# Kernel tuning notes

Measured on AMD Instinct MI355X. Metric: run time of the kernel, lower is better.

Reference implementation:

```python
import jax, jax.numpy as jnp
from jax import lax
import numpy as np


def conv4d(x, w, b, pad):
    """4D conv (stride 1) as a sum of 3D convs over the first-spatial-dim kernel taps.
    x: [B, Cin, T, D, H, W]; w: [Cout, Cin, Kt, Kd, Kh, Kw]; same pad on all dims."""
    B, Cin, T, D, H, W = x.shape
    Cout, _, Kt = w.shape[:3]
    xp = jnp.pad(x, ((0, 0), (0, 0), (pad, pad), (0, 0), (0, 0), (0, 0)))
    Tout = T + 2 * pad - Kt + 1
    acc = None
    for k in range(Kt):  # loop over kernel taps (<=3), not data dims
        xs = xp[:, :, k:k + Tout]                      # [B,Cin,Tout,D,H,W]
        xs = xs.transpose(0, 2, 1, 3, 4, 5).reshape(B * Tout, Cin, D, H, W)
        y = lax.conv_general_dilated(
            xs, w[:, :, k], (1, 1, 1), [(pad, pad)] * 3,
            dimension_numbers=('NCDHW', 'OIDHW', 'NCDHW'))
        acc = y if acc is None else acc + y
    Do, Ho, Wo = acc.shape[2:]
    out = acc.reshape(B, Tout, Cout, Do, Ho, Wo).transpose(0, 2, 1, 3, 4, 5)
    return out + b[None, :, None, None, None, None]


def tconv4d_k2s2(x, w, b):
    """4D transposed conv, kernel=2, stride=2, pad=0 (non-overlapping blocks).
    x: [B,Cin,T,D,H,W]; w: [Cin,Cout,2,2,2,2] (PyTorch ConvTranspose layout)."""
    B, Cin, T, D, H, W = x.shape
    Cout = w.shape[1]
    y = jnp.einsum('bcijkl,copqrs->boipjqkrls', x, w)
    y = y.reshape(B, Cout, 2 * T, 2 * D, 2 * H, 2 * W)
    return y + b[None, :, None, None, None, None]


def setup_inputs() -> dict:
    key = jax.random.key(0)
    ks = jax.random.split(key, 10)
    Cin, Cout = 64, 32
    x1 = jax.random.normal(ks[0], (2, Cin, 8, 8, 8, 8), dtype=jnp.float32)
    x2 = jax.random.normal(ks[1], (2, Cin // 2, 16, 16, 16, 16), dtype=jnp.float32)
    def w(k, shape, fan_in):
        return jax.random.normal(k, shape, dtype=jnp.float32) / np.float32(np.sqrt(fan_in))
    up_w = w(ks[2], (Cin, Cin // 2, 2, 2, 2, 2), Cin * 16)
    up_b = w(ks[3], (Cin // 2,), Cin * 16)
    w1 = w(ks[4], (Cout, Cin, 3, 3, 3, 3), Cin * 81)
    b1 = w(ks[5], (Cout,), Cin * 81)
    w2 = w(ks[6], (Cout, Cout, 3, 3, 3, 3), Cout * 81)
    b2 = w(ks[7], (Cout,), Cout * 81)
    w3 = w(ks[8], (Cout, Cin, 1, 1, 1, 1), Cin)
    b3 = w(ks[9], (Cout,), Cin)
    return {'x1': x1, 'x2': x2, 'up_w': up_w, 'up_b': up_b,
            'w1': w1, 'b1': b1, 'w2': w2, 'b2': b2, 'w3': w3, 'b3': b3}


def reference(x1, x2, up_w, up_b, w1, b1, w2, b2, w3, b3):
    x1u = tconv4d_k2s2(x1, up_w, up_b)              # [B, Cin//2, 16,16,16,16]
    xc = jnp.concatenate([x2, x1u], axis=1)          # [B, Cin, 16,16,16,16]
    Y = jax.nn.relu(conv4d(xc, w1, b1, 1))
    Y = conv4d(Y, w2, b2, 1)
    sc = conv4d(xc, w3, b3, 0)                       # 1x1 residual projection
    return jax.nn.relu(Y + sc)
```

## Files before the change

kernel.cpp:

```cpp
#include <hip/hip_runtime.h>

typedef unsigned short u16;
typedef __attribute__((ext_vector_type(8))) short short8;
typedef __attribute__((ext_vector_type(4))) float f32x4;

#define XCB_OFF  0
#define Y1B_OFF  8388608
#define W1P_OFF  12582912
#define W2P_OFF  12748800
#define W3P_OFF  12831744
#define UPWP_OFF 12833792
#define X1T_OFF  12866560

__device__ __forceinline__ u16 f2bf(float v) {
    unsigned u = __builtin_bit_cast(unsigned, v);
    u += 0x7FFFu + ((u >> 16) & 1u);
    return (u16)(u >> 16);
}

__device__ __forceinline__ f32x4 MFMA(short8 a, short8 b, f32x4 c) {
    return __builtin_amdgcn_mfma_f32_16x16x32_bf16(a, b, c, 0, 0, 0);
}

__device__ __forceinline__ void decode_bid(int bid, int& b, int& t, int& d, int& h0) {
    int xcd = bid & 7, loc = bid >> 3;
    int hB = loc & 1;
    d = (loc >> 1) & 15;
    int tsub = (loc >> 5) & 1;
    b = loc >> 6;
    t = xcd * 2 + tsub;
    h0 = hB * 8;
}

__global__ __launch_bounds__(256) void setup(const float* __restrict__ w1,
                                             const float* __restrict__ w2,
                                             const float* __restrict__ w3,
                                             const float* __restrict__ upw,
                                             const float* __restrict__ x1,
                                             const float* __restrict__ x2,
                                             u16* __restrict__ ws) {
    __shared__ u16 lds[256 * 72];
    int bid = blockIdx.x;
    int tid = threadIdx.x;
    if (bid < 32) {
        int b = bid >> 4;
        int pos_base = (bid & 15) * 256;
        u16* x1t = ws + X1T_OFF;
        #pragma unroll
        for (int c = 0; c < 64; ++c) {
            lds[tid * 72 + c] = f2bf(x1[((b * 64 + c) << 12) + pos_base + tid]);
        }
        __syncthreads();
        #pragma unroll
        for (int k = 0; k < 8; ++k) {
            int f = k * 256 + tid;
            int u = f & 7, pos = f >> 3;
            uint4 v = *(const uint4*)(lds + pos * 72 + u * 8);
            *(uint4*)(x1t + (size_t)((b << 12) + pos_base + pos) * 64 + u * 8) = v;
        }
    } else if (bid < 544) {
        int lb = bid - 32;
        int b = lb >> 8;
        int pos_base = (lb & 255) * 256;
        u16* xcb = ws + XCB_OFF;
        #pragma unroll
        for (int c = 0; c < 32; ++c) {
            lds[tid * 40 + c] = f2bf(x2[((b * 32 + c) << 16) + pos_base + tid]);
        }
        __syncthreads();
        #pragma unroll
        for (int k = 0; k < 4; ++k) {
            int f = k * 256 + tid;
            int u = f & 3, pos = f >> 2;
            uint4 v = *(const uint4*)(lds + pos * 40 + u * 8);
            *(uint4*)(xcb + (size_t)((b << 16) + pos_base + pos) * 64 + u * 8) = v;
        }
    } else {
        int idx = (bid - 544) * 256 + tid;
        if (idx < 165888) {
            int j = idx & 7, lane = (idx >> 3) & 63, rest = idx >> 9;
            int half = rest & 1, chunk = (rest >> 1) & 1, tap = rest >> 2;
            int co = half * 16 + (lane & 15), ci = chunk * 32 + (lane >> 4) * 8 + j;
            ws[W1P_OFF + idx] = f2bf(w1[(co * 64 + ci) * 81 + tap]);
        } else if (idx < 165888 + 82944) {
            int i2 = idx - 165888;
            int j = i2 & 7, lane = (i2 >> 3) & 63, rest = i2 >> 9;
            int half = rest & 1, tap = rest >> 1;
            int co = half * 16 + (lane & 15), ci = (lane >> 4) * 8 + j;
            ws[W2P_OFF + i2] = f2bf(w2[(co * 32 + ci) * 81 + tap]);
        } else if (idx < 165888 + 82944 + 2048) {
            int i3 = idx - (165888 + 82944);
            int j = i3 & 7, lane = (i3 >> 3) & 63, rest = i3 >> 9;
            int half = rest & 1, chunk = rest >> 1;
            int co = half * 16 + (lane & 15), ci = chunk * 32 + (lane >> 4) * 8 + j;
            ws[W3P_OFF + i3] = f2bf(w3[co * 64 + ci]);
        } else if (idx < 250880 + 32768) {
            int i4 = idx - 250880;
            int j = i4 & 7, lane = (i4 >> 3) & 63, rest = i4 >> 9;
            int half = rest & 1, chunk = (rest >> 1) & 1, tap = rest >> 2;
            int co = half * 16 + (lane & 15), ci = chunk * 32 + (lane >> 4) * 8 + j;
            ws[UPWP_OFF + i4] = f2bf(upw[(ci * 32 + co) * 16 + tap]);
        }
    }
}

__global__ __launch_bounds__(256) void xc_up_mfma(const u16* __restrict__ x1t,
                                                  const u16* __restrict__ upwp,
                                                  const float* __restrict__ up_b,
                                                  u16* __restrict__ xcb) {
    int tid = threadIdx.x;
    int wv = tid >> 6, lane = tid & 63;
    int q = lane >> 4, m = lane & 15;
    int wid = blockIdx.x * 4 + wv;
    int j = wid & 63, tap = (wid >> 6) & 15, b = wid >> 10;

    f32x4 acc[4][2];
    {
        float4 bi0 = ((const float4*)up_b)[q];
        float4 bi1 = ((const float4*)up_b)[4 + q];
        #pragma unroll
        for (int g = 0; g < 4; ++g) {
            acc[g][0] = (f32x4){bi0.x, bi0.y, bi0.z, bi0.w};
            acc[g][1] = (f32x4){bi1.x, bi1.y, bi1.z, bi1.w};
        }
    }

    const short8* wv8 = (const short8*)upwp;
    const u16* xb = x1t + (size_t)((b << 12) + (j << 6) + m) * 64;
    #pragma unroll
    for (int chunk = 0; chunk < 2; ++chunk) {
        short8 a0 = wv8[((tap * 2 + chunk) * 2 + 0) * 64 + lane];
        short8 a1 = wv8[((tap * 2 + chunk) * 2 + 1) * 64 + lane];
        #pragma unroll
        for (int g = 0; g < 4; ++g) {
            short8 bf = *(const short8*)(xb + (size_t)(g * 16) * 64 + chunk * 32 + q * 8);
            acc[g][0] = MFMA(a0, bf, acc[g][0]);
            acc[g][1] = MFMA(a1, bf, acc[g][1]);
        }
    }

    int it = j >> 3, id = j & 7;
    int pt = tap >> 3, pd = (tap >> 2) & 1, ph = (tap >> 1) & 1, pw = tap & 1;
    int oT = 2 * it + pt, oD = 2 * id + pd, oW = 2 * (m & 7) + pw;
    #pragma unroll
    for (int g = 0; g < 4; ++g) {
        int ih = g * 2 + (m >> 3);
        int opos = oT * 4096 + oD * 256 + (2 * ih + ph) * 16 + oW;
        u16* op = xcb + (size_t)((b << 16) + opos) * 64 + 32 + q * 4;
        #pragma unroll
        for (int half = 0; half < 2; ++half) {
            f32x4 v = acc[g][half];
            uint2 o;
            o.x = (unsigned)f2bf(v.x) | ((unsigned)f2bf(v.y) << 16);
            o.y = (unsigned)f2bf(v.z) | ((unsigned)f2bf(v.w) << 16);
            *(uint2*)(op + half * 16) = o;
        }
    }
}

__global__ __launch_bounds__(256, 4) void conv1_mfma(const u16* __restrict__ xcb,
                                                     const u16* __restrict__ w1p,
                                                     const float* __restrict__ b1,
                                                     u16* __restrict__ y1b) {
    __shared__ u16 lds[11520];
    int tid = threadIdx.x;
    int lane = tid & 63, wv = tid >> 6;
    int q = lane >> 4, m = lane & 15;
    int c = wv & 1, rg = wv >> 1;
    int b, t, d, h0;
    decode_bid(blockIdx.x, b, t, d, h0);
    int rot = (blockIdx.x * 5) % 9;

    int lofs[6], gofs[6];
    bool st[6], inr[6];
    #pragma unroll
    for (int k = 0; k < 6; ++k) {
        int ui = tid + k * 256;
        int u = ui & 7, p = (ui >> 3) % 18, hh = ui / 144;
        int gh = h0 - 1 + hh, gw = p - 1;
        st[k] = ui < 1440;
        inr[k] = st[k] && ((unsigned)gh < 16u) && ((unsigned)gw < 16u);
        gofs[k] = (gh * 16 + gw) * 64 + u * 8;
        lofs[k] = hh * 1152 + p * 64 + ((u ^ (p & 7)) * 8);
    }

    f32x4 acc[4][2];
    if (c == 0) {
        float4 bi0 = ((const float4*)b1)[q];
        float4 bi1 = ((const float4*)b1)[4 + q];
        #pragma unroll
        for (int i = 0; i < 4; ++i) {
            acc[i][0] = (f32x4){bi0.x, bi0.y, bi0.z, bi0.w};
            acc[i][1] = (f32x4){bi1.x, bi1.y, bi1.z, bi1.w};
        }
    } else {
        #pragma unroll
        for (int i = 0; i < 4; ++i) {
            acc[i][0] = (f32x4){0.f, 0.f, 0.f, 0.f};
            acc[i][1] = (f32x4){0.f, 0.f, 0.f, 0.f};
        }
    }
    const short8* w1v = (const short8*)w1p;

    uint4 rP[6];
    auto load_plane = [&](int ktd) {
        int kt = ktd / 3, kd = ktd - kt * 3;
        int tt = t + kt - 1, dd = d + kd - 1;
        bool pv = ((unsigned)tt < 16u) && ((unsigned)dd < 16u);
        const u16* src = xcb + (size_t)(((b * 16 + tt) * 16 + dd)) * 16384;
        #pragma unroll
        for (int k = 0; k < 6; ++k) {
            uint4 v = {0, 0, 0, 0};
            if (pv && inr[k]) v = *(const uint4*)(src + gofs[k]);
            rP[k] = v;
        }
    };
    auto write_plane = [&]() {
        #pragma unroll
        for (int k = 0; k < 6; ++k)
            if (st[k]) *(uint4*)(lds + lofs[k]) = rP[k];
    };

    load_plane(rot);
    for (int s = 0; s < 9; ++s) {
        int ktd = rot + s; if (ktd >= 9) ktd -= 9;
        __syncthreads();
        write_plane();
        if (s < 8) {
            int nk = ktd + 1; if (nk >= 9) nk -= 9;
            load_plane(nk);
        }
        __syncthreads();
        __builtin_amdgcn_s_setprio(1);
        #pragma unroll
        for (int kw = 0; kw < 3; ++kw) {
            int p = kw + m, pm = p & 7;
            int bo = p * 64 + ((((c << 2) | q) ^ pm) << 3);
            short8 R[6];
            #pragma unroll
            for (int r = 0; r < 6; ++r)
                R[r] = *(const short8*)(lds + (rg * 4 + r) * 1152 + bo);
            #pragma unroll
            for (int kh = 0; kh < 3; ++kh) {
                int tap = (ktd * 3 + kh) * 3 + kw;
                short8 a0 = w1v[((tap * 2 + c) * 2 + 0) * 64 + lane];
                short8 a1 = w1v[((tap * 2 + c) * 2 + 1) * 64 + lane];
                #pragma unroll
                for (int i = 0; i < 4; ++i) {
                    acc[i][0] = MFMA(a0, R[i + kh], acc[i][0]);
                    acc[i][1] = MFMA(a1, R[i + kh], acc[i][1]);
                }
            }
        }
        __builtin_amdgcn_s_setprio(0);
    }

    __syncthreads();
    f32x4* buf = (f32x4*)lds;
    if (c == 1) {
        #pragma unroll
        for (int i = 0; i < 4; ++i)
            #pragma unroll
            for (int half = 0; half < 2; ++half)
                buf[((rg * 4 + i) * 2 + half) * 64 + lane] = acc[i][half];
    }
    __syncthreads();
    if (c == 0) {
        int obase = ((b * 16 + t) * 16 + d) * 256 + (h0 + rg * 4) * 16 + m;
        #pragma unroll
        for (int i = 0; i < 4; ++i) {
            int pos = obase + i * 16;
            #pragma unroll
            for (int half = 0; half < 2; ++half) {
                f32x4 v = acc[i][half];
                f32x4 w = buf[((rg * 4 + i) * 2 + half) * 64 + lane];
                v.x += w.x; v.y += w.y; v.z += w.z; v.w += w.w;
                unsigned r0 = f2bf(fmaxf(v.x, 0.f)), r1 = f2bf(fmaxf(v.y, 0.f));
                unsigned r2 = f2bf(fmaxf(v.z, 0.f)), r3 = f2bf(fmaxf(v.w, 0.f));
                uint2 o;
                o.x = r0 | (r1 << 16);
                o.y = r2 | (r3 << 16);
                *(uint2*)(y1b + (size_t)pos * 32 + half * 16 + q * 4) = o;
            }
        }
    }
}

__global__ __launch_bounds__(256, 2) void conv2_mfma(const u16* __restrict__ y1b,
                                                     const u16* __restrict__ xcb,
                                                     const u16* __restrict__ w2p,
                                                     const u16* __restrict__ w3p,
                                                     const float* __restrict__ b2,
                                                     const float* __restrict__ b3,
                                                     float* __restrict__ out) {
    __shared__ u16 lds[2][10368];
    int tid = threadIdx.x;
    int lane = tid & 63, wv = tid >> 6;
    int q = lane >> 4, m = lane & 15;
    int rg = wv;
    int bid = blockIdx.x;
    int xcd = bid & 7, loc = bid >> 3;
    int d = loc & 15;
    int tsub = (loc >> 4) & 1;
    int b = loc >> 5;
    int t = xcd * 2 + tsub;
    int rot = (bid * 5) % 9;

    int lofs[6], gofs[6];
    bool st[6], inr[6];
    #pragma unroll
    for (int k = 0; k < 6; ++k) {
        int ui = tid + k * 256;
        int u = ui & 3, p = (ui >> 2) % 18, hh = ui / 72;
        int gh = hh - 1, gw = p - 1;
        st[k] = ui < 1296;
        inr[k] = st[k] && ((unsigned)gh < 16u) && ((unsigned)gw < 16u);
        gofs[k] = (gh * 16 + gw) * 32 + u * 8;
        lofs[k] = hh * 576 + p * 32 + ((u ^ (p & 3)) * 8);
    }

    f32x4 acc[4][2];
    {
        #pragma unroll
        for (int hf = 0; hf < 2; ++hf) {
            float4 p0 = ((const float4*)b2)[hf * 4 + q];
            float4 s0 = ((const float4*)b3)[hf * 4 + q];
            #pragma unroll
            for (int i = 0; i < 4; ++i)
                acc[i][hf] = (f32x4){p0.x + s0.x, p0.y + s0.y, p0.z + s0.z, p0.w + s0.w};
        }
    }
    const short8* w2v = (const short8*)w2p;

    uint4 rP[6];
    auto load_plane = [&](int ktd) {
        int kt = ktd / 3, kd = ktd - kt * 3;
        int tt = t + kt - 1, dd = d + kd - 1;
        bool pv = ((unsigned)tt < 16u) && ((unsigned)dd < 16u);
        const u16* src = y1b + (size_t)(((b * 16 + tt) * 16 + dd)) * 8192;
        #pragma unroll
        for (int k = 0; k < 6; ++k) {
            uint4 v = {0, 0, 0, 0};
            if (pv && inr[k]) v = *(const uint4*)(src + gofs[k]);
            rP[k] = v;
        }
    };
    auto write_plane = [&](int bb) {
        #pragma unroll
        for (int k = 0; k < 6; ++k)
            if (st[k]) *(uint4*)(&lds[bb][lofs[k]]) = rP[k];
    };

    load_plane(rot);
    write_plane(0);
    { int nk = rot + 1; if (nk >= 9) nk -= 9; load_plane(nk); }

    for (int s = 0; s < 9; ++s) {
        int ktd = rot + s; if (ktd >= 9) ktd -= 9;
        __syncthreads();
        const u16* L = lds[s & 1];
        __builtin_amdgcn_s_setprio(1);
        #pragma unroll
        for (int kw = 0; kw < 3; ++kw) {
            int p = kw + m, pm = p & 3;
            int bo = p * 32 + ((q ^ pm) << 3);
            short8 R[6];
            #pragma unroll
            for (int r = 0; r < 6; ++r)
                R[r] = *(const short8*)(L + (rg * 4 + r) * 576 + bo);
            #pragma unroll
            for (int kh = 0; kh < 3; ++kh) {
                int tap = (ktd * 3 + kh) * 3 + kw;
                short8 a0 = w2v[(tap * 2 + 0) * 64 + lane];
                short8 a1 = w2v[(tap * 2 + 1) * 64 + lane];
                #pragma unroll
                for (int i = 0; i < 4; ++i) {
                    acc[i][0] = MFMA(a0, R[i + kh], acc[i][0]);
                    acc[i][1] = MFMA(a1, R[i + kh], acc[i][1]);
                }
            }
        }
        __builtin_amdgcn_s_setprio(0);
        if (s < 8) {
            write_plane((s + 1) & 1);
            if (s < 7) {
                int nk = ktd + 2; if (nk >= 9) nk -= 9;
                load_plane(nk);
            }
        }
    }

    const short8* w3v = (const short8*)w3p;
    int lpos0 = (t * 16 + d) * 256 + (rg * 4) * 16 + m;
    int gpos0 = (b << 16) + lpos0;
    #pragma unroll
    for (int chunk = 0; chunk < 2; ++chunk) {
        short8 a0 = w3v[(chunk * 2 + 0) * 64 + lane];
        short8 a1 = w3v[(chunk * 2 + 1) * 64 + lane];
        #pragma unroll
        for (int i = 0; i < 4; ++i) {
            short8 bf = *(const short8*)(xcb + (size_t)(gpos0 + i * 16) * 64 + ((chunk << 2) | q) * 8);
            acc[i][0] = MFMA(a0, bf, acc[i][0]);
            acc[i][1] = MFMA(a1, bf, acc[i][1]);
        }
    }

    #pragma unroll
    for (int i = 0; i < 4; ++i) {
        int lpos = lpos0 + i * 16;
        #pragma unroll
        for (int hf = 0; hf < 2; ++hf) {
            f32x4 v = acc[i][hf];
            int co = hf * 16 + q * 4;
            float* op = out + (((size_t)(b * 32 + co)) << 16) + lpos;
            op[0ull << 16] = fmaxf(v.x, 0.f);
            op[1ull << 16] = fmaxf(v.y, 0.f);
            op[2ull << 16] = fmaxf(v.z, 0.f);
            op[3ull << 16] = fmaxf(v.w, 0.f);
        }
    }
}

extern "C" void kernel_launch(void* const* d_in, const int* in_sizes, int n_in,
                              void* d_out, int out_size, void* d_ws, size_t ws_size,
                              hipStream_t stream) {
    const float* x1   = (const float*)d_in[0];
    const float* x2   = (const float*)d_in[1];
    const float* up_w = (const float*)d_in[2];
    const float* up_b = (const float*)d_in[3];
    const float* w1   = (const float*)d_in[4];
    const float* b1   = (const float*)d_in[5];
    const float* w2   = (const float*)d_in[6];
    const float* b2   = (const float*)d_in[7];
    const float* w3   = (const float*)d_in[8];
    const float* b3   = (const float*)d_in[9];
    u16* ws  = (u16*)d_ws;
    float* out = (float*)d_out;

    setup<<<1652, 256, 0, stream>>>(w1, w2, w3, up_w, x1, x2, ws);
    xc_up_mfma<<<512, 256, 0, stream>>>(ws + X1T_OFF, ws + UPWP_OFF, up_b, ws + XCB_OFF);
    conv1_mfma<<<1024, 256, 0, stream>>>(ws + XCB_OFF, ws + W1P_OFF, b1, ws + Y1B_OFF);
    conv2_mfma<<<512, 256, 0, stream>>>(ws + Y1B_OFF, ws + XCB_OFF, ws + W2P_OFF,
                                        ws + W3P_OFF, b2, b3, out);
}
```

Baseline: 159.1 us.

## Use direct global-to-LDS loads with double buffering and fuse x1 transpose into upsample

The conv1 and conv2 plane staging now uses global_load_lds, which writes straight into a double-buffered LDS tile. A zero-padding buffer serves as the source for out-of-range taps, and the swizzle moves from the LDS address to the global source offset. This drops the register round trip and one barrier per step in conv1, and lets the next plane load overlap compute. The x1 bf16 transpose pass is removed from setup and done in LDS inside the upsample kernel, which now handles two taps per wave. Occupancy hints change (conv1 from 4 to 3, conv2 from 2 to 3), and conv1 doubles its LDS to hold two buffers.

```diff
diff --git a/kernel.cpp b/kernel.cpp
--- a/kernel.cpp
+++ b/kernel.cpp
@@ -10,7 +10,7 @@
 #define W2P_OFF  12748800
 #define W3P_OFF  12831744
 #define UPWP_OFF 12833792
-#define X1T_OFF  12866560
+#define ZPAD_OFF 12866560
 
 __device__ __forceinline__ u16 f2bf(float v) {
     unsigned u = __builtin_bit_cast(unsigned, v);
@@ -20,6 +20,12 @@
 
 __device__ __forceinline__ f32x4 MFMA(short8 a, short8 b, f32x4 c) {
     return __builtin_amdgcn_mfma_f32_16x16x32_bf16(a, b, c, 0, 0, 0);
+}
+
+typedef const __attribute__((address_space(1))) u16 gas_u16;
+typedef __attribute__((address_space(3))) u16 las_u16;
+__device__ __forceinline__ void gload16(const u16* g, u16* l) {
+    __builtin_amdgcn_global_load_lds((gas_u16*)g, (las_u16*)l, 16, 0, 0);
 }
 
 __device__ __forceinline__ void decode_bid(int bid, int& b, int& t, int& d, int& h0) {
@@ -36,32 +42,15 @@
                                              const float* __restrict__ w2,
                                              const float* __restrict__ w3,
                                              const float* __restrict__ upw,
-                                             const float* __restrict__ x1,
                                              const float* __restrict__ x2,
                                              u16* __restrict__ ws) {
-    __shared__ u16 lds[256 * 72];
+    __shared__ u16 lds[256 * 40];
     int bid = blockIdx.x;
     int tid = threadIdx.x;
-    if (bid < 32) {
-        int b = bid >> 4;
-        int pos_base = (bid & 15) * 256;
-        u16* x1t = ws + X1T_OFF;
-        #pragma unroll
-        for (int c = 0; c < 64; ++c) {
-            lds[tid * 72 + c] = f2bf(x1[((b * 64 + c) << 12) + pos_base + tid]);
-        }
-        __syncthreads();
-        #pragma unroll
-        for (int k = 0; k < 8; ++k) {
-            int f = k * 256 + tid;
-            int u = f & 7, pos = f >> 3;
-            uint4 v = *(const uint4*)(lds + pos * 72 + u * 8);
-            *(uint4*)(x1t + (size_t)((b << 12) + pos_base + pos) * 64 + u * 8) = v;
-        }
-    } else if (bid < 544) {
-        int lb = bid - 32;
-        int b = lb >> 8;
-        int pos_base = (lb & 255) * 256;
+    if (bid == 0 && tid < 64) ws[ZPAD_OFF + tid] = 0;
+    if (bid < 512) {
+        int b = bid >> 8;
+        int pos_base = (bid & 255) * 256;
         u16* xcb = ws + XCB_OFF;
         #pragma unroll
         for (int c = 0; c < 32; ++c) {
@@ -76,7 +65,7 @@
             *(uint4*)(xcb + (size_t)((b << 16) + pos_base + pos) * 64 + u * 8) = v;
         }
     } else {
-        int idx = (bid - 544) * 256 + tid;
+        int idx = (bid - 512) * 256 + tid;
         if (idx < 165888) {
             int j = idx & 7, lane = (idx >> 3) & 63, rest = idx >> 9;
             int half = rest & 1, chunk = (rest >> 1) & 1, tap = rest >> 2;
@@ -104,65 +93,74 @@
     }
 }
 
-__global__ __launch_bounds__(256) void xc_up_mfma(const u16* __restrict__ x1t,
+__global__ __launch_bounds__(256) void xc_up_mfma(const float* __restrict__ x1,
                                                   const u16* __restrict__ upwp,
                                                   const float* __restrict__ up_b,
                                                   u16* __restrict__ xcb) {
+    __shared__ u16 lds[64 * 72];
     int tid = threadIdx.x;
     int wv = tid >> 6, lane = tid & 63;
     int q = lane >> 4, m = lane & 15;
-    int wid = blockIdx.x * 4 + wv;
-    int j = wid & 63, tap = (wid >> 6) & 15, b = wid >> 10;
-
-    f32x4 acc[4][2];
-    {
-        float4 bi0 = ((const float4*)up_b)[q];
-        float4 bi1 = ((const float4*)up_b)[4 + q];
+    int bid = blockIdx.x;
+    int tp = bid & 1, j = (bid >> 1) & 63, b = bid >> 7;
+    int pos_base = j * 64;
+
+    #pragma unroll
+    for (int g = 0; g < 16; ++g) {
+        int c = g * 4 + wv;
+        lds[lane * 72 + c] = f2bf(x1[((b * 64 + c) << 12) + pos_base + lane]);
+    }
+    __syncthreads();
+
+    const short8* wv8 = (const short8*)upwp;
+    float4 bi0 = ((const float4*)up_b)[q];
+    float4 bi1 = ((const float4*)up_b)[4 + q];
+    int it = j >> 3, id = j & 7;
+
+    for (int tt = 0; tt < 2; ++tt) {
+        int tap = tp * 8 + wv * 2 + tt;
+        f32x4 acc[4][2];
         #pragma unroll
         for (int g = 0; g < 4; ++g) {
             acc[g][0] = (f32x4){bi0.x, bi0.y, bi0.z, bi0.w};
             acc[g][1] = (f32x4){bi1.x, bi1.y, bi1.z, bi1.w};
         }
-    }
-
-    const short8* wv8 = (const short8*)upwp;
-    const u16* xb = x1t + (size_t)((b << 12) + (j << 6) + m) * 64;
-    #pragma unroll
-    for (int chunk = 0; chunk < 2; ++chunk) {
-        short8 a0 = wv8[((tap * 2 + chunk) * 2 + 0) * 64 + lane];
-        short8 a1 = wv8[((tap * 2 + chunk) * 2 + 1) * 64 + lane];
+        #pragma unroll
+        for (int chunk = 0; chunk < 2; ++chunk) {
+            short8 a0 = wv8[((tap * 2 + chunk) * 2 + 0) * 64 + lane];
+            short8 a1 = wv8[((tap * 2 + chunk) * 2 + 1) * 64 + lane];
+            #pragma unroll
+            for (int g = 0; g < 4; ++g) {
+                short8 bf = *(const short8*)(lds + (g * 16 + m) * 72 + chunk * 32 + q * 8);
+                acc[g][0] = MFMA(a0, bf, acc[g][0]);
+                acc[g][1] = MFMA(a1, bf, acc[g][1]);
+            }
+        }
+        int pt = tap >> 3, pd = (tap >> 2) & 1, ph = (tap >> 1) & 1, pw = tap & 1;
+        int oT = 2 * it + pt, oD = 2 * id + pd, oW = 2 * (m & 7) + pw;
         #pragma unroll
         for (int g = 0; g < 4; ++g) {
-            short8 bf = *(const short8*)(xb + (size_t)(g * 16) * 64 + chunk * 32 + q * 8);
-            acc[g][0] = MFMA(a0, bf, acc[g][0]);
-            acc[g][1] = MFMA(a1, bf, acc[g][1]);
-        }
-    }
-
-    int it = j >> 3, id = j & 7;
-    int pt = tap >> 3, pd = (tap >> 2) & 1, ph = (tap >> 1) & 1, pw = tap & 1;
-    int oT = 2 * it + pt, oD = 2 * id + pd, oW = 2 * (m & 7) + pw;
-    #pragma unroll
-    for (int g = 0; g < 4; ++g) {
-        int ih = g * 2 + (m >> 3);
-        int opos = oT * 4096 + oD * 256 + (2 * ih + ph) * 16 + oW;
-        u16* op = xcb + (size_t)((b << 16) + opos) * 64 + 32 + q * 4;
-        #pragma unroll
-        for (int half = 0; half < 2; ++half) {
-            f32x4 v = acc[g][half];
-            uint2 o;
-            o.x = (unsigned)f2bf(v.x) | ((unsigned)f2bf(v.y) << 16);
-            o.y = (unsigned)f2bf(v.z) | ((unsigned)f2bf(v.w) << 16);
-            *(uint2*)(op + half * 16) = o;
-        }
-    }
-}
-
-__global__ __launch_bounds__(256, 4) void conv1_mfma(const u16* __restrict__ xcb,
+            int ih = g * 2 + (m >> 3);
+            int opos = oT * 4096 + oD * 256 + (2 * ih + ph) * 16 + oW;
+            u16* op = xcb + (size_t)((b << 16) + opos) * 64 + 32 + q * 4;
+            #pragma unroll
+            for (int half = 0; half < 2; ++half) {
+                f32x4 v = acc[g][half];
+                uint2 o;
+                o.x = (unsigned)f2bf(v.x) | ((unsigned)f2bf(v.y) << 16);
+                o.y = (unsigned)f2bf(v.z) | ((unsigned)f2bf(v.w) << 16);
+                *(uint2*)(op + half * 16) = o;
+            }
+        }
+    }
+}
+
+__global__ __launch_bounds__(256, 3) void conv1_mfma(const u16* __restrict__ xcb,
                                                      const u16* __restrict__ w1p,
                                                      const float* __restrict__ b1,
+                                                     const u16* __restrict__ zpad,
                                                      u16* __restrict__ y1b) {
-    __shared__ u16 lds[11520];
+    __shared__ __attribute__((aligned(16))) u16 lds[23040];
     int tid = threadIdx.x;
     int lane = tid & 63, wv = tid >> 6;
     int q = lane >> 4, m = lane & 15;
@@ -171,17 +169,19 @@
     decode_bid(blockIdx.x, b, t, d, h0);
     int rot = (blockIdx.x * 5) % 9;
 
-    int lofs[6], gofs[6];
+    int gofs[6], lofs[6];
     bool st[6], inr[6];
     #pragma unroll
     for (int k = 0; k < 6; ++k) {
         int ui = tid + k * 256;
-        int u = ui & 7, p = (ui >> 3) % 18, hh = ui / 144;
+        int hh = ui / 144, rem = ui - hh * 144;
+        int p = rem >> 3, w = rem & 7;
+        int u_src = w ^ (p & 7);
         int gh = h0 - 1 + hh, gw = p - 1;
         st[k] = ui < 1440;
         inr[k] = st[k] && ((unsigned)gh < 16u) && ((unsigned)gw < 16u);
-        gofs[k] = (gh * 16 + gw) * 64 + u * 8;
-        lofs[k] = hh * 1152 + p * 64 + ((u ^ (p & 7)) * 8);
+        gofs[k] = (gh * 16 + gw) * 64 + u_src * 8;
+        lofs[k] = ui * 8;
     }
 
     f32x4 acc[4][2];
@@ -202,35 +202,29 @@
     }
     const short8* w1v = (const short8*)w1p;
 
-    uint4 rP[6];
-    auto load_plane = [&](int ktd) {
+    auto issue_plane = [&](int ktd, int bb) {
         int kt = ktd / 3, kd = ktd - kt * 3;
         int tt = t + kt - 1, dd = d + kd - 1;
         bool pv = ((unsigned)tt < 16u) && ((unsigned)dd < 16u);
         const u16* src = xcb + (size_t)(((b * 16 + tt) * 16 + dd)) * 16384;
         #pragma unroll
         for (int k = 0; k < 6; ++k) {
-            uint4 v = {0, 0, 0, 0};
-            if (pv && inr[k]) v = *(const uint4*)(src + gofs[k]);
-            rP[k] = v;
+            if (st[k]) {
+                const u16* g = (pv && inr[k]) ? (src + gofs[k]) : zpad;
+                gload16(g, lds + bb * 11520 + lofs[k]);
+            }
         }
     };
-    auto write_plane = [&]() {
-        #pragma unroll
-        for (int k = 0; k < 6; ++k)
-            if (st[k]) *(uint4*)(lds + lofs[k]) = rP[k];
-    };
-
-    load_plane(rot);
+
+    issue_plane(rot, 0);
     for (int s = 0; s < 9; ++s) {
         int ktd = rot + s; if (ktd >= 9) ktd -= 9;
         __syncthreads();
-        write_plane();
         if (s < 8) {
             int nk = ktd + 1; if (nk >= 9) nk -= 9;
-            load_plane(nk);
-        }
-        __syncthreads();
+            issue_plane(nk, (s + 1) & 1);
+        }
+        const u16* L = lds + (s & 1) * 11520;
         __builtin_amdgcn_s_setprio(1);
         #pragma unroll
         for (int kw = 0; kw < 3; ++kw) {
@@ -239,7 +233,7 @@
             short8 R[6];
             #pragma unroll
             for (int r = 0; r < 6; ++r)
-                R[r] = *(const short8*)(lds + (rg * 4 + r) * 1152 + bo);
+                R[r] = *(const short8*)(L + (rg * 4 + r) * 1152 + bo);
             #pragma unroll
             for (int kh = 0; kh < 3; ++kh) {
                 int tap = (ktd * 3 + kh) * 3 + kw;
@@ -286,14 +280,15 @@
     }
 }
 
-__global__ __launch_bounds__(256, 2) void conv2_mfma(const u16* __restrict__ y1b,
+__global__ __launch_bounds__(256, 3) void conv2_mfma(const u16* __restrict__ y1b,
                                                      const u16* __restrict__ xcb,
                                                      const u16* __restrict__ w2p,
                                                      const u16* __restrict__ w3p,
                                                      const float* __restrict__ b2,
                                                      const float* __restrict__ b3,
+                                                     const u16* __restrict__ zpad,
                                                      float* __restrict__ out) {
-    __shared__ u16 lds[2][10368];
+    __shared__ __attribute__((aligned(16))) u16 lds[20736];
     int tid = threadIdx.x;
     int lane = tid & 63, wv = tid >> 6;
     int q = lane >> 4, m = lane & 15;
@@ -306,59 +301,55 @@
     int t = xcd * 2 + tsub;
     int rot = (bid * 5) % 9;
 
-    int lofs[6], gofs[6];
+    int gofs[6], lofs[6];
     bool st[6], inr[6];
     #pragma unroll
     for (int k = 0; k < 6; ++k) {
         int ui = tid + k * 256;
-        int u = ui & 3, p = (ui >> 2) % 18, hh = ui / 72;
+        int hh = ui / 72, rem = ui - hh * 72;
+        int p = rem >> 2, w = rem & 3;
+        int u_src = w ^ (p & 3);
         int gh = hh - 1, gw = p - 1;
         st[k] = ui < 1296;
         inr[k] = st[k] && ((unsigned)gh < 16u) && ((unsigned)gw < 16u);
-        gofs[k] = (gh * 16 + gw) * 32 + u * 8;
-        lofs[k] = hh * 576 + p * 32 + ((u ^ (p & 3)) * 8);
+        gofs[k] = (gh * 16 + gw) * 32 + u_src * 8;
+        lofs[k] = ui * 8;
     }
 
     f32x4 acc[4][2];
-    {
-        #pragma unroll
-        for (int hf = 0; hf < 2; ++hf) {
-            float4 p0 = ((const float4*)b2)[hf * 4 + q];
-            float4 s0 = ((const float4*)b3)[hf * 4 + q];
-            #pragma unroll
-            for (int i = 0; i < 4; ++i)
-                acc[i][hf] = (f32x4){p0.x + s0.x, p0.y + s0.y, p0.z + s0.z, p0.w + s0.w};
-        }
+    #pragma unroll
+    for (int hf = 0; hf < 2; ++hf) {
+        float4 p0 = ((const float4*)b2)[hf * 4 + q];
+        float4 s0 = ((const float4*)b3)[hf * 4 + q];
+        #pragma unroll
+        for (int i = 0; i < 4; ++i)
+            acc[i][hf] = (f32x4){p0.x + s0.x, p0.y + s0.y, p0.z + s0.z, p0.w + s0.w};
     }
     const short8* w2v = (const short8*)w2p;
 
-    uint4 rP[6];
-    auto load_plane = [&](int ktd) {
+    auto issue_plane = [&](int ktd, int bb) {
         int kt = ktd / 3, kd = ktd - kt * 3;
         int tt = t + kt - 1, dd = d + kd - 1;
         bool pv = ((unsigned)tt < 16u) && ((unsigned)dd < 16u);
         const u16* src = y1b + (size_t)(((b * 16 + tt) * 16 + dd)) * 8192;
         #pragma unroll
         for (int k = 0; k < 6; ++k) {
-            uint4 v = {0, 0, 0, 0};
-            if (pv && inr[k]) v = *(const uint4*)(src + gofs[k]);
-            rP[k] = v;
+            if (st[k]) {
+                const u16* g = (pv && inr[k]) ? (src + gofs[k]) : zpad;
+                gload16(g, lds + bb * 10368 + lofs[k]);
+            }
         }
     };
-    auto write_plane = [&](int bb) {
-        #pragma unroll
-        for (int k = 0; k < 6; ++k)
-            if (st[k]) *(uint4*)(&lds[bb][lofs[k]]) = rP[k];
-    };
-
-    load_plane(rot);
-    write_plane(0);
-    { int nk = rot + 1; if (nk >= 9) nk -= 9; load_plane(nk); }
-
+
+    issue_plane(rot, 0);
     for (int s = 0; s < 9; ++s) {
         int ktd = rot + s; if (ktd >= 9) ktd -= 9;
         __syncthreads();
-        const u16* L = lds[s & 1];
+        if (s < 8) {
+            int nk = ktd + 1; if (nk >= 9) nk -= 9;
+            issue_plane(nk, (s + 1) & 1);
+        }
+        const u16* L = lds + (s & 1) * 10368;
         __builtin_amdgcn_s_setprio(1);
         #pragma unroll
         for (int kw = 0; kw < 3; ++kw) {
@@ -381,13 +372,6 @@
             }
         }
         __builtin_amdgcn_s_setprio(0);
-        if (s < 8) {
-            write_plane((s + 1) & 1);
-            if (s < 7) {
-                int nk = ktd + 2; if (nk >= 9) nk -= 9;
-                load_plane(nk);
-            }
-        }
     }
 
     const short8* w3v = (const short8*)w3p;
@@ -437,9 +421,10 @@
     u16* ws  = (u16*)d_ws;
     float* out = (float*)d_out;
 
-    setup<<<1652, 256, 0, stream>>>(w1, w2, w3, up_w, x1, x2, ws);
-    xc_up_mfma<<<512, 256, 0, stream>>>(ws + X1T_OFF, ws + UPWP_OFF, up_b, ws + XCB_OFF);
-    conv1_mfma<<<1024, 256, 0, stream>>>(ws + XCB_OFF, ws + W1P_OFF, b1, ws + Y1B_OFF);
+    setup<<<1620, 256, 0, stream>>>(w1, w2, w3, up_w, x2, ws);
+    xc_up_mfma<<<256, 256, 0, stream>>>(x1, ws + UPWP_OFF, up_b, ws + XCB_OFF);
+    conv1_mfma<<<1024, 256, 0, stream>>>(ws + XCB_OFF, ws + W1P_OFF, b1,
+                                         ws + ZPAD_OFF, ws + Y1B_OFF);
     conv2_mfma<<<512, 256, 0, stream>>>(ws + Y1B_OFF, ws + XCB_OFF, ws + W2P_OFF,
-                                        ws + W3P_OFF, b2, b3, out);
-}
+                                        ws + W3P_OFF, b2, b3, ws + ZPAD_OFF, out);
+}
```

Measured after the change: 162.9 us. +2.4%, slower.
